# Kernel tuning notes

Measured on AMD Instinct MI355X. Metric: run time of the kernel, lower is better.

Reference implementation:

```python
import jax, jax.numpy as jnp
import numpy as np


def conv1x1(x, w, b):
    # x: [b,c,h,w], w: [o,c], b: [o]
    return jnp.einsum('bchw,oc->bohw', x, w) + b[None, :, None, None]


def maxpool2(x):
    b, c, h, w = x.shape
    return x.reshape(b, c, h // 2, 2, w // 2, 2).max(axis=(3, 5))


def setup_inputs() -> dict:
    key = jax.random.key(0)
    ks = jax.random.split(key, 10)
    c = 64
    x = jax.random.normal(ks[0], (16, c, 64, 64), dtype=jnp.float32)
    s = 0.05
    wf = jax.random.normal(ks[1], (c // 8, c), dtype=jnp.float32) * s
    bf = jax.random.normal(ks[2], (c // 8,), dtype=jnp.float32) * s
    wg = jax.random.normal(ks[3], (c // 8, c), dtype=jnp.float32) * s
    bg = jax.random.normal(ks[4], (c // 8,), dtype=jnp.float32) * s
    wh = jax.random.normal(ks[5], (c // 2, c), dtype=jnp.float32) * s
    bh = jax.random.normal(ks[6], (c // 2,), dtype=jnp.float32) * s
    wv = jax.random.normal(ks[7], (c, c // 2), dtype=jnp.float32) * s
    bv = jax.random.normal(ks[8], (c,), dtype=jnp.float32) * s
    gamma = jax.random.normal(ks[9], (1,), dtype=jnp.float32)
    return {'x': x, 'wf': wf, 'bf': bf, 'wg': wg, 'bg': bg,
            'wh': wh, 'bh': bh, 'wv': wv, 'bv': bv, 'gamma': gamma}


def reference(x, wf, bf, wg, bg, wh, bh, wv, bv, gamma):
    b, c, h, w = x.shape
    n = h * w          # query length
    m = n // 4         # key/value length after 2x2 maxpool
    # query branch: f(x) -> [b, c//8, n]
    fx = conv1x1(x, wf, bf).reshape(b, c // 8, n)
    # key branch: maxpool(g(x)) -> [b, c//8, m]
    gx = maxpool2(conv1x1(x, wg, bg)).reshape(b, c // 8, m)
    # attention: [b, n, m]
    attn = jax.nn.softmax(jnp.einsum('bcn,bcm->bnm', fx, gx), axis=-1)
    # value branch: maxpool(h(x)) -> [b, c//2, m]
    hx = maxpool2(conv1x1(x, wh, bh)).reshape(b, c // 2, m)
    # merge: [b, c//2, n] -> [b, c//2, h, w]
    merged = jnp.einsum('bnm,bcm->bcn', attn, hx).reshape(b, c // 2, h, w)
    return x + gamma[0] * conv1x1(merged, wv, bv)
```

## Files before the change

kernel.cpp:

```cpp
#include <hip/hip_runtime.h>
#include <hip/hip_bf16.h>
#include <math.h>

#define BB 16
#define CC 64
#define HW 4096
#define MM 1024
#define CK 8
#define CV 32
#define LOG2E 1.4426950408889634f

typedef float f32x4 __attribute__((ext_vector_type(4)));
typedef short s16x8 __attribute__((ext_vector_type(8)));

union U4 { uint4 u; s16x8 s; };

__device__ inline unsigned short bfu(float a) {
    __hip_bfloat16 h = __float2bfloat16(a);
    union { __hip_bfloat16 h; unsigned short u; } c; c.h = h; return c.u;
}
__device__ inline unsigned int pk2bf(float a, float b) {
    return (unsigned int)bfu(a) | ((unsigned int)bfu(b) << 16);
}
__device__ inline unsigned int pk2bf_t(float a, float b) {
    return (__float_as_uint(a) >> 16) | (__float_as_uint(b) & 0xffff0000u);
}

__device__ inline float hwexp2(float s) {
#if __has_builtin(__builtin_amdgcn_exp2f)
    return __builtin_amdgcn_exp2f(s);
#else
    float r;
    asm volatile("v_exp_f32 %0, %1\n\ts_nop 1" : "=v"(r) : "v"(s));
    return r;
#endif
}

#define FXB_OFF 0
#define GXA_OFF 1048576
#define HXC_OFF 1310720
#define WVB_OFF 2359296
#define FRG_OFF 2363392

__global__ __launch_bounds__(256, 6) void prep_kernel(
    const float* __restrict__ x,
    const float* __restrict__ wf, const float* __restrict__ bf,
    const float* __restrict__ wg, const float* __restrict__ bg,
    const float* __restrict__ wh, const float* __restrict__ bh,
    const float* __restrict__ wv,
    unsigned short* __restrict__ fxB, unsigned short* __restrict__ gxA,
    unsigned short* __restrict__ hxC, unsigned short* __restrict__ wvB)
{
    __shared__ __align__(16) float wsm[8 * CC];
    __shared__ __align__(16) unsigned short sHp[64][8];

    int tid   = threadIdx.x;
    int chunk = blockIdx.y;
    const float* wsrc = (chunk == 0) ? wf : (chunk == 1) ? wg : (wh + (size_t)(chunk - 2) * 8 * CC);
    const float* bsrc = (chunk == 0) ? bf : (chunk == 1) ? bg : (bh + (chunk - 2) * 8);

    for (int i = tid; i < 8 * CC; i += 256) wsm[i] = wsrc[i];

    if (blockIdx.x == 0 && chunk == 0) {
        int t = tid >> 6, ll = tid & 63;
        const float* wr = wv + (size_t)(t * 16 + (ll & 15)) * CV + ((ll >> 4) * 8);
        uint4 wu;
        wu.x = pk2bf(wr[0], wr[1]); wu.y = pk2bf(wr[2], wr[3]);
        wu.z = pk2bf(wr[4], wr[5]); wu.w = pk2bf(wr[6], wr[7]);
        *(uint4*)(wvB + (size_t)tid * 8) = wu;
    }
    __syncthreads();

    int wave = tid >> 6, l = tid & 63;
    int wp = blockIdx.x * 4 + wave;
    int b  = wp >> 6;
    int t2 = wp & 63;
    int rpair = t2 >> 1, chalf = t2 & 1;
    int col = chalf * 32 + (l >> 2) * 2 + (l & 1);
    int row = rpair * 2 + ((l >> 1) & 1);
    int pix = row * 64 + col;

    float o8[8];
#pragma unroll
    for (int o = 0; o < 8; ++o) o8[o] = bsrc[o];

    const float* xp = x + (size_t)b * CC * HW + pix;
#pragma unroll 4
    for (int c4 = 0; c4 < CC; c4 += 4) {
        float v0 = xp[(c4 + 0) * HW];
        float v1 = xp[(c4 + 1) * HW];
        float v2 = xp[(c4 + 2) * HW];
        float v3 = xp[(c4 + 3) * HW];
#pragma unroll
        for (int o = 0; o < 8; ++o) {
            float4 w = *(const float4*)&wsm[o * CC + c4];
            o8[o] = fmaf(w.x, v0, fmaf(w.y, v1, fmaf(w.z, v2, fmaf(w.w, v3, o8[o]))));
        }
    }

    if (chunk == 0) {
        uint4 fu;
        fu.x = pk2bf(o8[0] * LOG2E, o8[1] * LOG2E);
        fu.y = pk2bf(o8[2] * LOG2E, o8[3] * LOG2E);
        fu.z = pk2bf(o8[4] * LOG2E, o8[5] * LOG2E);
        fu.w = pk2bf(o8[6] * LOG2E, o8[7] * LOG2E);
        *(uint4*)(fxB + (size_t)(b * HW + pix) * CK) = fu;
    } else {
#pragma unroll
        for (int o = 0; o < 8; ++o) {
            o8[o] = fmaxf(o8[o], __shfl_xor(o8[o], 1, 64));
            o8[o] = fmaxf(o8[o], __shfl_xor(o8[o], 2, 64));
        }
        int ppl = l >> 2;
        if (chunk == 1) {
            if ((l & 3) == 0) {
                uint4 gu;
                gu.x = pk2bf(o8[0], o8[1]); gu.y = pk2bf(o8[2], o8[3]);
                gu.z = pk2bf(o8[4], o8[5]); gu.w = pk2bf(o8[6], o8[7]);
                *(uint4*)(gxA + (size_t)(b * MM + t2 * 16 + ppl) * CK) = gu;
            }
        } else {
            if ((l & 3) == 0) {
                uint4 hu;
                hu.x = pk2bf(o8[0], o8[1]); hu.y = pk2bf(o8[2], o8[3]);
                hu.z = pk2bf(o8[4], o8[5]); hu.w = pk2bf(o8[6], o8[7]);
                *(uint4*)&sHp[wave * 16 + ppl][0] = hu;
            }
            __syncthreads();
            int ch = tid >> 5, j = tid & 31;
            unsigned int v = (unsigned int)sHp[2 * j][ch]
                           | ((unsigned int)sHp[2 * j + 1][ch] << 16);
            int ppb = (blockIdx.x * 4 & 63) * 16;
            int chg = (chunk - 2) * 8 + ch;
            *(unsigned int*)(hxC + (size_t)(b * CV + chg) * MM + ppb + 2 * j) = v;
        }
    }
}

__global__ __launch_bounds__(256) void tile_kernel(
    const unsigned short* __restrict__ gxA, const unsigned short* __restrict__ hxC,
    unsigned short* __restrict__ frag)
{
    int bg = blockIdx.x;
    int b  = bg >> 5, g = bg & 31;
    int tid = threadIdx.x;
    int which = tid >> 6, l = tid & 63;
    int q16 = l & 15, h = l >> 4;
    int prm = ((q16 & 12) << 1) | (q16 & 3);

    const unsigned short* src;
    if (which < 2) {
        src = gxA + (size_t)(b * MM + g * 32 + prm + (which ? 4 : 0)) * CK;
    } else {
        src = hxC + (size_t)(b * CV + prm + ((which == 3) ? 4 : 0)) * MM + g * 32 + h * 8;
    }
    uint4 v = *(const uint4*)src;
    *(uint4*)(frag + ((size_t)bg * 4 + which) * 64 * 8 + (size_t)l * 8) = v;
}

__global__ __launch_bounds__(512, 4) void attn_kernel(
    const float* __restrict__ x,
    const unsigned short* __restrict__ fxB, const unsigned short* __restrict__ frag,
    const unsigned short* __restrict__ wvB,
    const float* __restrict__ bv, const float* __restrict__ gamma,
    float* __restrict__ out)
{
    __shared__ float sAcc[2][4][8][64];
    __shared__ float sSum[2][4][64];

    int tid = threadIdx.x;
    int l   = tid & 63;
    int w   = tid >> 6;
    int qh  = w & 1;
    int kq  = w >> 1;
    int b   = blockIdx.x >> 7;
    int qb  = (blockIdx.x & 127) * 32;
    int q16 = l & 15;
    int h   = l >> 4;
    bool lo16 = (l < 16);

    U4 qf;
    {
        uint4 v = *(const uint4*)(fxB + (size_t)(b * HW + qb + qh * 16 + q16) * CK);
        if (!lo16) { v.x = 0; v.y = 0; v.z = 0; v.w = 0; }
        qf.u = v;
    }

    f32x4 zz = {0.f, 0.f, 0.f, 0.f};
    f32x4 acc0 = zz, acc1 = zz;
    float ssum = 0.f;

    const unsigned short* fb = frag + ((size_t)(b * 32 + kq * 8) * 4) * 64 * 8
                                    + (size_t)l * 8;

#pragma unroll 2
    for (int gi = 0; gi < 8; ++gi) {
        U4 ga, gb2, v0, v1;
        ga.u  = *(const uint4*)(fb + 0 * 512);
        gb2.u = *(const uint4*)(fb + 1 * 512);
        v0.u  = *(const uint4*)(fb + 2 * 512);
        v1.u  = *(const uint4*)(fb + 3 * 512);
        fb += 2048;

        f32x4 s0 = __builtin_amdgcn_mfma_f32_16x16x32_bf16(ga.s,  qf.s, zz, 0, 0, 0);
        f32x4 s1 = __builtin_amdgcn_mfma_f32_16x16x32_bf16(gb2.s, qf.s, zz, 0, 0, 0);
        float e0 = hwexp2(s0.x), e1 = hwexp2(s0.y), e2 = hwexp2(s0.z), e3 = hwexp2(s0.w);
        float e4 = hwexp2(s1.x), e5 = hwexp2(s1.y), e6 = hwexp2(s1.z), e7 = hwexp2(s1.w);
        ssum += ((e0 + e1) + (e2 + e3)) + ((e4 + e5) + (e6 + e7));
        U4 bp;
        bp.u.x = pk2bf_t(e0, e1); bp.u.y = pk2bf_t(e2, e3);
        bp.u.z = pk2bf_t(e4, e5); bp.u.w = pk2bf_t(e6, e7);
        acc0 = __builtin_amdgcn_mfma_f32_16x16x32_bf16(v0.s, bp.s, acc0, 0, 0, 0);
        acc1 = __builtin_amdgcn_mfma_f32_16x16x32_bf16(v1.s, bp.s, acc1, 0, 0, 0);
    }

#pragma unroll
    for (int e = 0; e < 4; ++e) {
        sAcc[qh][kq][e][l]     = acc0[e];
        sAcc[qh][kq][4 + e][l] = acc1[e];
    }
    sSum[qh][kq][l] = ssum;
    __syncthreads();

    int qt_f = w & 1;
    int ot   = w >> 1;
    f32x4 ca0 = zz, ca1 = zz;
    float cs = 0.f;
#pragma unroll
    for (int k2 = 0; k2 < 4; ++k2) {
#pragma unroll
        for (int e = 0; e < 4; ++e) {
            ca0[e] += sAcc[qt_f][k2][e][l];
            ca1[e] += sAcc[qt_f][k2][4 + e][l];
        }
        cs += sSum[qt_f][k2][l];
    }
    cs += __shfl_xor(cs, 16, 64);
    cs += __shfl_xor(cs, 32, 64);
    float inv = 1.0f / cs;

    U4 mb;
    mb.u.x = pk2bf_t(ca0.x * inv, ca0.y * inv);
    mb.u.y = pk2bf_t(ca0.z * inv, ca0.w * inv);
    mb.u.z = pk2bf_t(ca1.x * inv, ca1.y * inv);
    mb.u.w = pk2bf_t(ca1.z * inv, ca1.w * inv);

    float gm = gamma[0];
    int q = qb + qt_f * 16 + q16;
    const float* xq = x + (size_t)b * CC * HW + q;
    float*       oq = out + (size_t)b * CC * HW + q;
    U4 wva;
    wva.u = *(const uint4*)(wvB + (size_t)(ot * 64 + l) * CK);
    f32x4 d = __builtin_amdgcn_mfma_f32_16x16x32_bf16(wva.s, mb.s, zz, 0, 0, 0);
#pragma unroll
    for (int r = 0; r < 4; ++r) {
        int o = ot * 16 + h * 4 + r;
        oq[(size_t)o * HW] = xq[(size_t)o * HW] + gm * (d[r] + bv[o]);
    }
}

extern "C" void kernel_launch(void* const* d_in, const int* in_sizes, int n_in,
                              void* d_out, int out_size, void* d_ws, size_t ws_size,
                              hipStream_t stream) {
    const float* x     = (const float*)d_in[0];
    const float* wf    = (const float*)d_in[1];
    const float* bf    = (const float*)d_in[2];
    const float* wg    = (const float*)d_in[3];
    const float* bg    = (const float*)d_in[4];
    const float* wh    = (const float*)d_in[5];
    const float* bh    = (const float*)d_in[6];
    const float* wv    = (const float*)d_in[7];
    const float* bv    = (const float*)d_in[8];
    const float* gamma = (const float*)d_in[9];
    float* out = (float*)d_out;
    char* ws = (char*)d_ws;

    unsigned short* fxB  = (unsigned short*)(ws + FXB_OFF);
    unsigned short* gxA  = (unsigned short*)(ws + GXA_OFF);
    unsigned short* hxC  = (unsigned short*)(ws + HXC_OFF);
    unsigned short* wvB  = (unsigned short*)(ws + WVB_OFF);
    unsigned short* frag = (unsigned short*)(ws + FRG_OFF);

    prep_kernel<<<dim3(256, 6), 256, 0, stream>>>(x, wf, bf, wg, bg, wh, bh, wv,
                                                  fxB, gxA, hxC, wvB);
    tile_kernel<<<512, 256, 0, stream>>>(gxA, hxC, frag);
    attn_kernel<<<2048, 512, 0, stream>>>(x, fxB, frag, wvB, bv, gamma, out);
}
```

Measured before the change: 46.25 us.

## Process two query tiles per wave to reuse key/value fragment loads

Each wave now handles two 16-query tiles instead of one, so every loaded key and value fragment feeds twice as many MFMAs, and each block covers 64 queries with half the grid. This is meant to halve global fragment traffic per query and amortize load latency. The cost is more registers per wave (four accumulators, two sets of exponentials), larger shared memory, and fewer blocks to spread across CUs.

```diff
diff --git a/kernel.cpp b/kernel.cpp
--- a/kernel.cpp
+++ b/kernel.cpp
@@ -165,30 +165,33 @@
     const float* __restrict__ bv, const float* __restrict__ gamma,
     float* __restrict__ out)
 {
-    __shared__ float sAcc[2][4][8][64];
-    __shared__ float sSum[2][4][64];
+    __shared__ float sAcc[4][4][8][64];
+    __shared__ float sSum[4][4][64];
 
     int tid = threadIdx.x;
     int l   = tid & 63;
     int w   = tid >> 6;
-    int qh  = w & 1;
-    int kq  = w >> 1;
-    int b   = blockIdx.x >> 7;
-    int qb  = (blockIdx.x & 127) * 32;
+    int qg  = w >> 2;
+    int kq  = w & 3;
+    int b   = blockIdx.x >> 6;
+    int qb  = (blockIdx.x & 63) * 64;
     int q16 = l & 15;
     int h   = l >> 4;
     bool lo16 = (l < 16);
 
-    U4 qf;
+    U4 qf0, qf1;
     {
-        uint4 v = *(const uint4*)(fxB + (size_t)(b * HW + qb + qh * 16 + q16) * CK);
+        uint4 v = *(const uint4*)(fxB + (size_t)(b * HW + qb + (qg * 2 + 0) * 16 + q16) * CK);
         if (!lo16) { v.x = 0; v.y = 0; v.z = 0; v.w = 0; }
-        qf.u = v;
+        qf0.u = v;
+        uint4 v2 = *(const uint4*)(fxB + (size_t)(b * HW + qb + (qg * 2 + 1) * 16 + q16) * CK);
+        if (!lo16) { v2.x = 0; v2.y = 0; v2.z = 0; v2.w = 0; }
+        qf1.u = v2;
     }
 
     f32x4 zz = {0.f, 0.f, 0.f, 0.f};
-    f32x4 acc0 = zz, acc1 = zz;
-    float ssum = 0.f;
+    f32x4 a00 = zz, a01 = zz, a10 = zz, a11 = zz;
+    float ssum0 = 0.f, ssum1 = 0.f;
 
     const unsigned short* fb = frag + ((size_t)(b * 32 + kq * 8) * 4) * 64 * 8
                                     + (size_t)l * 8;
@@ -202,28 +205,46 @@
         v1.u  = *(const uint4*)(fb + 3 * 512);
         fb += 2048;
 
-        f32x4 s0 = __builtin_amdgcn_mfma_f32_16x16x32_bf16(ga.s,  qf.s, zz, 0, 0, 0);
-        f32x4 s1 = __builtin_amdgcn_mfma_f32_16x16x32_bf16(gb2.s, qf.s, zz, 0, 0, 0);
+        f32x4 s0 = __builtin_amdgcn_mfma_f32_16x16x32_bf16(ga.s,  qf0.s, zz, 0, 0, 0);
+        f32x4 s1 = __builtin_amdgcn_mfma_f32_16x16x32_bf16(gb2.s, qf0.s, zz, 0, 0, 0);
+        f32x4 t0 = __builtin_amdgcn_mfma_f32_16x16x32_bf16(ga.s,  qf1.s, zz, 0, 0, 0);
+        f32x4 t1 = __builtin_amdgcn_mfma_f32_16x16x32_bf16(gb2.s, qf1.s, zz, 0, 0, 0);
+
         float e0 = hwexp2(s0.x), e1 = hwexp2(s0.y), e2 = hwexp2(s0.z), e3 = hwexp2(s0.w);
         float e4 = hwexp2(s1.x), e5 = hwexp2(s1.y), e6 = hwexp2(s1.z), e7 = hwexp2(s1.w);
-        ssum += ((e0 + e1) + (e2 + e3)) + ((e4 + e5) + (e6 + e7));
-        U4 bp;
-        bp.u.x = pk2bf_t(e0, e1); bp.u.y = pk2bf_t(e2, e3);
-        bp.u.z = pk2bf_t(e4, e5); bp.u.w = pk2bf_t(e6, e7);
-        acc0 = __builtin_amdgcn_mfma_f32_16x16x32_bf16(v0.s, bp.s, acc0, 0, 0, 0);
-        acc1 = __builtin_amdgcn_mfma_f32_16x16x32_bf16(v1.s, bp.s, acc1, 0, 0, 0);
-    }
-
-#pragma unroll
-    for (int e = 0; e < 4; ++e) {
-        sAcc[qh][kq][e][l]     = acc0[e];
-        sAcc[qh][kq][4 + e][l] = acc1[e];
-    }
-    sSum[qh][kq][l] = ssum;
+        float f0 = hwexp2(t0.x), f1 = hwexp2(t0.y), f2 = hwexp2(t0.z), f3 = hwexp2(t0.w);
+        float f4 = hwexp2(t1.x), f5 = hwexp2(t1.y), f6 = hwexp2(t1.z), f7 = hwexp2(t1.w);
+        ssum0 += ((e0 + e1) + (e2 + e3)) + ((e4 + e5) + (e6 + e7));
+        ssum1 += ((f0 + f1) + (f2 + f3)) + ((f4 + f5) + (f6 + f7));
+
+        U4 bp0, bp1;
+        bp0.u.x = pk2bf_t(e0, e1); bp0.u.y = pk2bf_t(e2, e3);
+        bp0.u.z = pk2bf_t(e4, e5); bp0.u.w = pk2bf_t(e6, e7);
+        bp1.u.x = pk2bf_t(f0, f1); bp1.u.y = pk2bf_t(f2, f3);
+        bp1.u.z = pk2bf_t(f4, f5); bp1.u.w = pk2bf_t(f6, f7);
+
+        a00 = __builtin_amdgcn_mfma_f32_16x16x32_bf16(v0.s, bp0.s, a00, 0, 0, 0);
+        a01 = __builtin_amdgcn_mfma_f32_16x16x32_bf16(v1.s, bp0.s, a01, 0, 0, 0);
+        a10 = __builtin_amdgcn_mfma_f32_16x16x32_bf16(v0.s, bp1.s, a10, 0, 0, 0);
+        a11 = __builtin_amdgcn_mfma_f32_16x16x32_bf16(v1.s, bp1.s, a11, 0, 0, 0);
+    }
+
+    {
+        int qt0 = qg * 2, qt1 = qg * 2 + 1;
+#pragma unroll
+        for (int e = 0; e < 4; ++e) {
+            sAcc[qt0][kq][e][l]     = a00[e];
+            sAcc[qt0][kq][4 + e][l] = a01[e];
+            sAcc[qt1][kq][e][l]     = a10[e];
+            sAcc[qt1][kq][4 + e][l] = a11[e];
+        }
+        sSum[qt0][kq][l] = ssum0;
+        sSum[qt1][kq][l] = ssum1;
+    }
     __syncthreads();
 
-    int qt_f = w & 1;
-    int ot   = w >> 1;
+    int qt_f = w & 3;
+    int oth  = w >> 2;
     f32x4 ca0 = zz, ca1 = zz;
     float cs = 0.f;
 #pragma unroll
@@ -249,13 +270,17 @@
     int q = qb + qt_f * 16 + q16;
     const float* xq = x + (size_t)b * CC * HW + q;
     float*       oq = out + (size_t)b * CC * HW + q;
-    U4 wva;
-    wva.u = *(const uint4*)(wvB + (size_t)(ot * 64 + l) * CK);
-    f32x4 d = __builtin_amdgcn_mfma_f32_16x16x32_bf16(wva.s, mb.s, zz, 0, 0, 0);
-#pragma unroll
-    for (int r = 0; r < 4; ++r) {
-        int o = ot * 16 + h * 4 + r;
-        oq[(size_t)o * HW] = xq[(size_t)o * HW] + gm * (d[r] + bv[o]);
+#pragma unroll
+    for (int i = 0; i < 2; ++i) {
+        int ot = oth * 2 + i;
+        U4 wva;
+        wva.u = *(const uint4*)(wvB + (size_t)(ot * 64 + l) * CK);
+        f32x4 d = __builtin_amdgcn_mfma_f32_16x16x32_bf16(wva.s, mb.s, zz, 0, 0, 0);
+#pragma unroll
+        for (int r = 0; r < 4; ++r) {
+            int o = ot * 16 + h * 4 + r;
+            oq[(size_t)o * HW] = xq[(size_t)o * HW] + gm * (d[r] + bv[o]);
+        }
     }
 }
 
@@ -284,5 +309,5 @@
     prep_kernel<<<dim3(256, 6), 256, 0, stream>>>(x, wf, bf, wg, bg, wh, bh, wv,
                                                   fxB, gxA, hxC, wvB);
     tile_kernel<<<512, 256, 0, stream>>>(gxA, hxC, frag);
-    attn_kernel<<<2048, 512, 0, stream>>>(x, fxB, frag, wvB, bv, gamma, out);
-}
+    attn_kernel<<<1024, 512, 0, stream>>>(x, fxB, frag, wvB, bv, gamma, out);
+}
```

Result: faster. 42.84 us (-7.4%).

## Process four query tiles per wave to reuse key/value fragments

Applied to the files above, without the earlier changes.

Each block now covers 64 queries instead of 32, and every wave loops over four 16-query tiles while splitting the key range eight ways, so each loaded key/value fragment serves four query tiles. This cuts global fragment loads per query and halves the grid. In exchange it needs more registers for accumulators and more shared memory (about 72KB), which may lower occupancy under the 512-thread launch bound. The output stage now has each wave do two output tiles.

```diff
diff --git a/kernel.cpp b/kernel.cpp
--- a/kernel.cpp
+++ b/kernel.cpp
@@ -165,36 +165,37 @@
     const float* __restrict__ bv, const float* __restrict__ gamma,
     float* __restrict__ out)
 {
-    __shared__ float sAcc[2][4][8][64];
-    __shared__ float sSum[2][4][64];
+    __shared__ float sAcc[4][8][8][64];
+    __shared__ float sSum[4][8][64];
 
     int tid = threadIdx.x;
     int l   = tid & 63;
     int w   = tid >> 6;
-    int qh  = w & 1;
-    int kq  = w >> 1;
-    int b   = blockIdx.x >> 7;
-    int qb  = (blockIdx.x & 127) * 32;
+    int b   = blockIdx.x >> 6;
+    int qb  = (blockIdx.x & 63) * 64;
     int q16 = l & 15;
     int h   = l >> 4;
     bool lo16 = (l < 16);
 
-    U4 qf;
-    {
-        uint4 v = *(const uint4*)(fxB + (size_t)(b * HW + qb + qh * 16 + q16) * CK);
+    U4 qf[4];
+#pragma unroll
+    for (int t = 0; t < 4; ++t) {
+        uint4 v = *(const uint4*)(fxB + (size_t)(b * HW + qb + t * 16 + q16) * CK);
         if (!lo16) { v.x = 0; v.y = 0; v.z = 0; v.w = 0; }
-        qf.u = v;
+        qf[t].u = v;
     }
 
     f32x4 zz = {0.f, 0.f, 0.f, 0.f};
-    f32x4 acc0 = zz, acc1 = zz;
-    float ssum = 0.f;
-
-    const unsigned short* fb = frag + ((size_t)(b * 32 + kq * 8) * 4) * 64 * 8
+    f32x4 acc[4][2];
+#pragma unroll
+    for (int t = 0; t < 4; ++t) { acc[t][0] = zz; acc[t][1] = zz; }
+    float ssum[4] = {0.f, 0.f, 0.f, 0.f};
+
+    const unsigned short* fb = frag + ((size_t)(b * 32 + w * 4) * 4) * 64 * 8
                                     + (size_t)l * 8;
 
 #pragma unroll 2
-    for (int gi = 0; gi < 8; ++gi) {
+    for (int gi = 0; gi < 4; ++gi) {
         U4 ga, gb2, v0, v1;
         ga.u  = *(const uint4*)(fb + 0 * 512);
         gb2.u = *(const uint4*)(fb + 1 * 512);
@@ -202,32 +203,38 @@
         v1.u  = *(const uint4*)(fb + 3 * 512);
         fb += 2048;
 
-        f32x4 s0 = __builtin_amdgcn_mfma_f32_16x16x32_bf16(ga.s,  qf.s, zz, 0, 0, 0);
-        f32x4 s1 = __builtin_amdgcn_mfma_f32_16x16x32_bf16(gb2.s, qf.s, zz, 0, 0, 0);
-        float e0 = hwexp2(s0.x), e1 = hwexp2(s0.y), e2 = hwexp2(s0.z), e3 = hwexp2(s0.w);
-        float e4 = hwexp2(s1.x), e5 = hwexp2(s1.y), e6 = hwexp2(s1.z), e7 = hwexp2(s1.w);
-        ssum += ((e0 + e1) + (e2 + e3)) + ((e4 + e5) + (e6 + e7));
-        U4 bp;
-        bp.u.x = pk2bf_t(e0, e1); bp.u.y = pk2bf_t(e2, e3);
-        bp.u.z = pk2bf_t(e4, e5); bp.u.w = pk2bf_t(e6, e7);
-        acc0 = __builtin_amdgcn_mfma_f32_16x16x32_bf16(v0.s, bp.s, acc0, 0, 0, 0);
-        acc1 = __builtin_amdgcn_mfma_f32_16x16x32_bf16(v1.s, bp.s, acc1, 0, 0, 0);
-    }
-
-#pragma unroll
-    for (int e = 0; e < 4; ++e) {
-        sAcc[qh][kq][e][l]     = acc0[e];
-        sAcc[qh][kq][4 + e][l] = acc1[e];
-    }
-    sSum[qh][kq][l] = ssum;
+#pragma unroll
+        for (int t = 0; t < 4; ++t) {
+            f32x4 s0 = __builtin_amdgcn_mfma_f32_16x16x32_bf16(ga.s,  qf[t].s, zz, 0, 0, 0);
+            f32x4 s1 = __builtin_amdgcn_mfma_f32_16x16x32_bf16(gb2.s, qf[t].s, zz, 0, 0, 0);
+            float e0 = hwexp2(s0.x), e1 = hwexp2(s0.y), e2 = hwexp2(s0.z), e3 = hwexp2(s0.w);
+            float e4 = hwexp2(s1.x), e5 = hwexp2(s1.y), e6 = hwexp2(s1.z), e7 = hwexp2(s1.w);
+            ssum[t] += ((e0 + e1) + (e2 + e3)) + ((e4 + e5) + (e6 + e7));
+            U4 bp;
+            bp.u.x = pk2bf_t(e0, e1); bp.u.y = pk2bf_t(e2, e3);
+            bp.u.z = pk2bf_t(e4, e5); bp.u.w = pk2bf_t(e6, e7);
+            acc[t][0] = __builtin_amdgcn_mfma_f32_16x16x32_bf16(v0.s, bp.s, acc[t][0], 0, 0, 0);
+            acc[t][1] = __builtin_amdgcn_mfma_f32_16x16x32_bf16(v1.s, bp.s, acc[t][1], 0, 0, 0);
+        }
+    }
+
+#pragma unroll
+    for (int t = 0; t < 4; ++t) {
+#pragma unroll
+        for (int e = 0; e < 4; ++e) {
+            sAcc[t][w][e][l]     = acc[t][0][e];
+            sAcc[t][w][4 + e][l] = acc[t][1][e];
+        }
+        sSum[t][w][l] = ssum[t];
+    }
     __syncthreads();
 
-    int qt_f = w & 1;
-    int ot   = w >> 1;
+    int qt_f = w >> 1;
+    int oth  = w & 1;
     f32x4 ca0 = zz, ca1 = zz;
     float cs = 0.f;
 #pragma unroll
-    for (int k2 = 0; k2 < 4; ++k2) {
+    for (int k2 = 0; k2 < 8; ++k2) {
 #pragma unroll
         for (int e = 0; e < 4; ++e) {
             ca0[e] += sAcc[qt_f][k2][e][l];
@@ -249,13 +256,17 @@
     int q = qb + qt_f * 16 + q16;
     const float* xq = x + (size_t)b * CC * HW + q;
     float*       oq = out + (size_t)b * CC * HW + q;
-    U4 wva;
-    wva.u = *(const uint4*)(wvB + (size_t)(ot * 64 + l) * CK);
-    f32x4 d = __builtin_amdgcn_mfma_f32_16x16x32_bf16(wva.s, mb.s, zz, 0, 0, 0);
-#pragma unroll
-    for (int r = 0; r < 4; ++r) {
-        int o = ot * 16 + h * 4 + r;
-        oq[(size_t)o * HW] = xq[(size_t)o * HW] + gm * (d[r] + bv[o]);
+#pragma unroll
+    for (int i = 0; i < 2; ++i) {
+        int ot = oth * 2 + i;
+        U4 wva;
+        wva.u = *(const uint4*)(wvB + (size_t)(ot * 64 + l) * CK);
+        f32x4 d = __builtin_amdgcn_mfma_f32_16x16x32_bf16(wva.s, mb.s, zz, 0, 0, 0);
+#pragma unroll
+        for (int r = 0; r < 4; ++r) {
+            int o = ot * 16 + h * 4 + r;
+            oq[(size_t)o * HW] = xq[(size_t)o * HW] + gm * (d[r] + bv[o]);
+        }
     }
 }
 
@@ -284,5 +295,5 @@
     prep_kernel<<<dim3(256, 6), 256, 0, stream>>>(x, wf, bf, wg, bg, wh, bh, wv,
                                                   fxB, gxA, hxC, wvB);
     tile_kernel<<<512, 256, 0, stream>>>(gxA, hxC, frag);
-    attn_kernel<<<2048, 512, 0, stream>>>(x, fxB, frag, wvB, bv, gamma, out);
-}
+    attn_kernel<<<1024, 512, 0, stream>>>(x, fxB, frag, wvB, bv, gamma, out);
+}
```

After: 42.71 us. 1.08x faster.
